# Kernel tuning notes

Hardware: AMD Instinct MI355X
Metric: run time of the kernel (lower is better)

The kernel has to match this reference:

```python
import jax, jax.numpy as jnp
import numpy as np

E = 1024   # embed_dim
H = 16     # num_heads
D = E // H # head_dim = 64
HD2 = D // 2
B = 2
S = 2048


def setup_inputs() -> dict:
    key = jax.random.key(0)
    ks = jax.random.split(key, 12)
    def lin(k, fan_in, fan_out):
        # xavier-uniform-ish init, stored in [in, out] (jax) convention
        lim = float(np.sqrt(6.0 / (fan_in + fan_out)))
        return jax.random.uniform(k, (fan_in, fan_out), jnp.float32, -lim, lim)
    return {
        "query": jax.random.normal(ks[0], (B, S, E), jnp.float32),
        "xi_scale": jax.random.uniform(ks[1], (B,), jnp.float32),
        "Wq": lin(ks[2], E, E), "bq": jnp.zeros((E,), jnp.float32),
        "Wk": lin(ks[3], E, E), "bk": jnp.zeros((E,), jnp.float32),
        "Wv": lin(ks[4], E, E), "bv": jnp.zeros((E,), jnp.float32),
        "Wo": lin(ks[5], E, E), "bo": jnp.zeros((E,), jnp.float32),
        "enc_w1": lin(ks[6], 1, HD2), "enc_b1": jnp.zeros((HD2,), jnp.float32),
        "ln_g": jnp.ones((HD2,), jnp.float32), "ln_b": jnp.zeros((HD2,), jnp.float32),
        "enc_w2": lin(ks[7], HD2, D), "enc_b2": jnp.zeros((D,), jnp.float32),
        "scale_gating": jnp.ones((H,), jnp.float32),
    }


def reference(query, xi_scale, Wq, bq, Wk, bk, Wv, bv, Wo, bo,
              enc_w1, enc_b1, ln_g, ln_b, enc_w2, enc_b2, scale_gating):
    b, s, e = query.shape
    h, d = H, e // H
    # --- scale adaptation: xi -> Linear -> LayerNorm -> GELU -> Linear ---
    x = xi_scale[:, None] @ enc_w1 + enc_b1                  # [B, D/2]
    mu = x.mean(-1, keepdims=True)
    var = ((x - mu) ** 2).mean(-1, keepdims=True)
    x = (x - mu) / jnp.sqrt(var + 1e-5) * ln_g + ln_b
    x = jax.nn.gelu(x, approximate=False)
    xe = x @ enc_w2 + enc_b2                                 # [B, D]
    adapt = 1.0 + jax.nn.sigmoid(scale_gating)[None, :, None] * xe[:, None, :]  # [B, H, D]
    # --- projections (self-attention: key = value = query) ---
    q = (query @ Wq + bq).reshape(b, s, h, d).transpose(0, 2, 1, 3) * adapt[:, :, None, :]
    k = (query @ Wk + bk).reshape(b, s, h, d).transpose(0, 2, 1, 3) * adapt[:, :, None, :]
    v = (query @ Wv + bv).reshape(b, s, h, d).transpose(0, 2, 1, 3)
    # --- explicit QK^T / sqrt(d) -> softmax -> V ---
    inv_scale = 1.0 / float(np.sqrt(d))
    scores = jnp.einsum('bhqd,bhkd->bhqk', q, k) * inv_scale  # [B, H, S, S]
    attn = jax.nn.softmax(scores, axis=-1)
    out = jnp.einsum('bhqk,bhkd->bhqd', attn, v)              # [B, H, S, D]
    out = out.transpose(0, 2, 1, 3).reshape(b, s, e)
    return out @ Wo + bo
```

## Files before the change

kernel.cpp:

```cpp
#include <hip/hip_runtime.h>

typedef __bf16 bf16;
typedef __attribute__((ext_vector_type(8))) __bf16 bf16x8;
typedef __attribute__((ext_vector_type(4))) float f32x4;
typedef __attribute__((ext_vector_type(16))) float f32x16;
typedef unsigned int u32;

#define MFMA16(a, b, c) __builtin_amdgcn_mfma_f32_16x16x32_bf16((a), (b), (c), 0, 0, 0)
#define MFMA32(a, b, c) __builtin_amdgcn_mfma_f32_32x32x16_bf16((a), (b), (c), 0, 0, 0)

#define BB 2
#define SS 2048
#define EE 1024
#define HH 16
#define DD 64
#define MM (BB * SS)

__device__ inline f32x4 zero4() {
    f32x4 z; z.x = 0.f; z.y = 0.f; z.z = 0.f; z.w = 0.f; return z;
}

__device__ __forceinline__ void gload16(const bf16* g, bf16* l) {
    __builtin_amdgcn_global_load_lds(
        (const __attribute__((address_space(1))) u32*)(const void*)g,
        (__attribute__((address_space(3))) u32*)(void*)l,
        16, 0, 0);
}

__device__ __forceinline__ u32 pkbf(float a, float b) {
    union { __bf16 h; unsigned short s; } ua, ub;
    ua.h = (__bf16)a; ub.h = (__bf16)b;
    return (u32)ua.s | ((u32)ub.s << 16);
}

__global__ __launch_bounds__(256) void prep_kernel(
    const float* __restrict__ query, bf16* __restrict__ qc,
    const float* __restrict__ s0, const float* __restrict__ s1,
    const float* __restrict__ s2, const float* __restrict__ s3,
    bf16* __restrict__ d0, bf16* __restrict__ d1,
    bf16* __restrict__ d2, bf16* __restrict__ d3,
    const float* __restrict__ xi, const float* __restrict__ w1,
    const float* __restrict__ b1, const float* __restrict__ lng,
    const float* __restrict__ lnb, const float* __restrict__ w2,
    const float* __restrict__ b2, const float* __restrict__ gate,
    float* __restrict__ adapt) {
    __shared__ bf16 tile[64 * 72];
    const int bid = blockIdx.x;
    const int t = threadIdx.x;

    if (bid < 2048) {
        const int i = (bid * 256 + t) * 8;
        float4 a = *(const float4*)(query + i);
        float4 b = *(const float4*)(query + i + 4);
        bf16 tmp[8];
        tmp[0] = (bf16)a.x; tmp[1] = (bf16)a.y; tmp[2] = (bf16)a.z; tmp[3] = (bf16)a.w;
        tmp[4] = (bf16)b.x; tmp[5] = (bf16)b.y; tmp[6] = (bf16)b.z; tmp[7] = (bf16)b.w;
        *(uint4*)(qc + i) = *(uint4*)tmp;
    } else if (bid < 3072) {
        const int m = (bid - 2048) >> 8;
        const int idx0 = (bid - 2048) & 255;
        const float* W = (m == 0) ? s0 : (m == 1) ? s1 : (m == 2) ? s2 : s3;
        bf16* Wt = (m == 0) ? d0 : (m == 1) ? d1 : (m == 2) ? d2 : d3;
        const int k0 = (idx0 >> 4) * 64, n0 = (idx0 & 15) * 64;
#pragma unroll
        for (int i = 0; i < 2; ++i) {
            int idx = i * 256 + t;
            int r = idx >> 3, c = (idx & 7) * 8;
            float4 a = *(const float4*)(W + (k0 + r) * EE + n0 + c);
            float4 b = *(const float4*)(W + (k0 + r) * EE + n0 + c + 4);
            bf16 tmp[8];
            tmp[0] = (bf16)a.x; tmp[1] = (bf16)a.y; tmp[2] = (bf16)a.z; tmp[3] = (bf16)a.w;
            tmp[4] = (bf16)b.x; tmp[5] = (bf16)b.y; tmp[6] = (bf16)b.z; tmp[7] = (bf16)b.w;
            *(uint4*)(tile + r * 72 + c) = *(uint4*)tmp;
        }
        __syncthreads();
#pragma unroll
        for (int i = 0; i < 2; ++i) {
            int idx = i * 256 + t;
            int n = idx >> 3, kc = (idx & 7) * 8;
            bf16 tmp[8];
#pragma unroll
            for (int j = 0; j < 8; ++j) tmp[j] = tile[(kc + j) * 72 + n];
            *(uint4*)(Wt + (n0 + n) * EE + k0 + kc) = *(uint4*)tmp;
        }
    } else {
        const int b = bid - 3072;
        float* xs = (float*)tile;
        if (t < 64) {
            const float xiv = xi[b];
            float xv = 0.f;
            if (t < 32) xv = xiv * w1[t] + b1[t];
            float sm = xv;
            for (int off = 1; off < 32; off <<= 1) sm += __shfl_xor(sm, off);
            const float mu = sm * (1.f / 32.f);
            float dv = (t < 32) ? (xv - mu) : 0.f;
            float s2 = dv * dv;
            for (int off = 1; off < 32; off <<= 1) s2 += __shfl_xor(s2, off);
            const float var = s2 * (1.f / 32.f);
            if (t < 32) {
                float xn = (xv - mu) * rsqrtf(var + 1e-5f) * lng[t] + lnb[t];
                float ge = 0.5f * xn * (1.f + erff(xn * 0.70710678118654752f));
                xs[t] = ge;
            }
        }
        __syncthreads();
        if (t < 64) {
            float acc = b2[t];
            for (int j = 0; j < 32; ++j) acc += xs[j] * w2[j * DD + t];
            for (int h = 0; h < HH; ++h) {
                float sg = 1.f / (1.f + __expf(-gate[h]));
                adapt[(b * HH + h) * DD + t] = 1.f + sg * acc;
            }
        }
    }
}

__global__ __launch_bounds__(256, 3) void gemm_qkv(
    const bf16* __restrict__ Aq, const bf16* __restrict__ Bqk,
    const bf16* __restrict__ Av,
    const float* __restrict__ bias, const float* __restrict__ bias2,
    const float* __restrict__ bias3, const float* __restrict__ adapt,
    bf16* __restrict__ outqk, bf16* __restrict__ outvt) {
    __shared__ bf16 As[2 * 128 * 32];
    __shared__ bf16 Bs[2 * 128 * 32];

    const int t = threadIdx.x;
    const int w = t >> 6, lane = t & 63;
    const int mrow = lane & 15, quad = lane >> 4;
    const int wm = (w & 1) * 64, wn = (w >> 1) * 64;

    int md, bx, by;
    const bf16 *Ap, *Bp;
    int bid = blockIdx.x;
    if (bid < 512) { md = 5; bx = bid & 31; by = bid >> 5; Ap = Aq; Bp = Bqk; }
    else { md = 4; bid -= 512; bx = bid & 7; by = bid >> 3; Ap = Av; Bp = Aq; }
    const int m0 = bx * 128, n0 = by * 128;

    f32x4 acc[4][4];
#pragma unroll
    for (int i = 0; i < 4; ++i)
#pragma unroll
        for (int j = 0; j < 4; ++j) acc[i][j] = zero4();

    const int dr = lane >> 2;
    const int dcg = ((lane & 3) ^ (dr & 3)) * 8;
    const bf16* Ag = Ap + (size_t)(m0 + w * 16 + dr) * EE + dcg;
    const bf16* Bg = Bp + (size_t)(n0 + w * 16 + dr) * EE + dcg;
    bf16* Al = As + (w * 16) * 32;
    bf16* Bl = Bs + (w * 16) * 32;

    gload16(Ag, Al);
    gload16(Ag + 64 * EE, Al + 64 * 32);
    gload16(Bg, Bl);
    gload16(Bg + 64 * EE, Bl + 64 * 32);

    for (int kt = 0; kt < 32; ++kt) {
        __syncthreads();
        if (kt < 31) {
            const int kn = (kt + 1) * 32;
            const int nb = (kt + 1) & 1;
            gload16(Ag + kn, Al + nb * 4096);
            gload16(Ag + 64 * EE + kn, Al + nb * 4096 + 64 * 32);
            gload16(Bg + kn, Bl + nb * 4096);
            gload16(Bg + 64 * EE + kn, Bl + nb * 4096 + 64 * 32);
        }
        const bf16* Ab = As + (kt & 1) * 4096;
        const bf16* Bb = Bs + (kt & 1) * 4096;
        const int sw = (quad ^ (mrow & 3)) * 8;
        bf16x8 af[4], bfr[4];
#pragma unroll
        for (int i = 0; i < 4; ++i)
            af[i] = *(const bf16x8*)(Ab + (wm + i * 16 + mrow) * 32 + sw);
#pragma unroll
        for (int j = 0; j < 4; ++j)
            bfr[j] = *(const bf16x8*)(Bb + (wn + j * 16 + mrow) * 32 + sw);
#pragma unroll
        for (int i = 0; i < 4; ++i)
#pragma unroll
            for (int j = 0; j < 4; ++j)
                acc[i][j] = MFMA16(af[i], bfr[j], acc[i][j]);
    }

#pragma unroll
    for (int i = 0; i < 4; ++i) {
#pragma unroll
        for (int j = 0; j < 4; ++j) {
            const int col = n0 + wn + j * 16 + mrow;
#pragma unroll
            for (int r = 0; r < 4; ++r) {
                const int row = m0 + wm + i * 16 + quad * 4 + r;
                float v = acc[i][j][r];
                if (md == 4) {
                    v += bias3[row];
                    const int h = row >> 6, d = row & 63;
                    const int b = col >> 11, s = col & (SS - 1);
                    outvt[(((b * HH + h) * DD + d) * SS) + s] = (bf16)v;
                } else {
                    const int m2 = col >> 10;
                    const int cl = col & 1023;
                    const int h = cl >> 6, d = cl & 63;
                    const int b = row >> 11, s = row & (SS - 1);
                    v += (m2 ? bias2[cl] : bias[cl]);
                    v *= adapt[(b * HH + h) * DD + d];
                    if (!m2) v *= 0.18033688011113811f;
                    outqk[(size_t)m2 * MM * EE + ((b * HH + h) * SS + s) * DD + d] = (bf16)v;
                }
            }
        }
    }
}

__global__ __launch_bounds__(256, 3) void gemm_o(
    const bf16* __restrict__ A, const bf16* __restrict__ Bt,
    const float* __restrict__ bias, float* __restrict__ outf) {
    __shared__ bf16 As[2 * 128 * 64];
    __shared__ bf16 Bs[2 * 64 * 64];

    const int t = threadIdx.x;
    const int w = t >> 6, lane = t & 63;
    const int mrow = lane & 15, quad = lane >> 4;
    const int m0 = blockIdx.x * 128, n0 = blockIdx.y * 64;

    f32x4 acc[2][4];
#pragma unroll
    for (int i = 0; i < 2; ++i)
#pragma unroll
        for (int j = 0; j < 4; ++j) acc[i][j] = zero4();

    const int grow = lane >> 3;
    const int gsw = ((lane & 7) ^ grow) * 8;
    const bf16* Ag = A + (size_t)(m0 + w * 32 + grow) * EE + gsw;
    const bf16* Bg = Bt + (size_t)(n0 + w * 16 + grow) * EE + gsw;
    bf16* Al = As + (w * 32) * 64;
    bf16* Bl = Bs + (w * 16) * 64;

#pragma unroll
    for (int i = 0; i < 4; ++i) gload16(Ag + i * 8 * EE, Al + i * 8 * 64);
#pragma unroll
    for (int i = 0; i < 2; ++i) gload16(Bg + i * 8 * EE, Bl + i * 8 * 64);

    for (int kt = 0; kt < 16; ++kt) {
        __syncthreads();
        if (kt < 15) {
            const int kn = (kt + 1) * 64;
            const int nb = (kt + 1) & 1;
#pragma unroll
            for (int i = 0; i < 4; ++i)
                gload16(Ag + i * 8 * EE + kn, Al + nb * 8192 + i * 8 * 64);
#pragma unroll
            for (int i = 0; i < 2; ++i)
                gload16(Bg + i * 8 * EE + kn, Bl + nb * 4096 + i * 8 * 64);
        }
        const bf16* Ab = As + (kt & 1) * 8192;
        const bf16* Bb = Bs + (kt & 1) * 4096;
#pragma unroll
        for (int ks = 0; ks < 2; ++ks) {
            const int cg = ks * 4 + quad;
            const int sw = (cg ^ (mrow & 7)) * 8;
            bf16x8 af[2], bfr[4];
#pragma unroll
            for (int mi = 0; mi < 2; ++mi)
                af[mi] = *(const bf16x8*)(Ab + (w * 32 + mi * 16 + mrow) * 64 + sw);
#pragma unroll
            for (int nj = 0; nj < 4; ++nj)
                bfr[nj] = *(const bf16x8*)(Bb + (nj * 16 + mrow) * 64 + sw);
#pragma unroll
            for (int mi = 0; mi < 2; ++mi)
#pragma unroll
                for (int nj = 0; nj < 4; ++nj)
                    acc[mi][nj] = MFMA16(af[mi], bfr[nj], acc[mi][nj]);
        }
    }

#pragma unroll
    for (int mi = 0; mi < 2; ++mi) {
#pragma unroll
        for (int nj = 0; nj < 4; ++nj) {
            const int col = n0 + nj * 16 + mrow;
#pragma unroll
            for (int r = 0; r < 4; ++r) {
                const int row = m0 + w * 32 + mi * 16 + quad * 4 + r;
                outf[row * EE + col] = acc[mi][nj][r] + bias[col];
            }
        }
    }
}

__global__ __launch_bounds__(256, 2) void attn_kernel(
    const bf16* __restrict__ q, const bf16* __restrict__ k,
    const bf16* __restrict__ vt, bf16* __restrict__ o0, bf16* __restrict__ o1,
    float* __restrict__ lws) {
    __shared__ bf16 lds[16896];
    bf16* Ks = lds;
    bf16* Vs = lds + 8192;

    const int t = threadIdx.x;
    const int w = t >> 6, lane = t & 63;
    const int q32 = lane & 31, h = lane >> 5;
    const int split = blockIdx.x >> 8;
    const int rest = blockIdx.x & 255;
    const int bh = rest >> 3;
    const int qb = rest & 7;
    const int qr0 = qb * 256 + w * 64;

    bf16x8 qf[2][4];
#pragma unroll
    for (int qi = 0; qi < 2; ++qi)
#pragma unroll
        for (int c = 0; c < 4; ++c)
            qf[qi][c] = *(const bf16x8*)(q + (size_t)(bh * SS + qr0 + qi * 32 + q32) * DD +
                                         c * 16 + h * 8);

    f32x16 oacc[2][2];
#pragma unroll
    for (int qi = 0; qi < 2; ++qi)
#pragma unroll
        for (int mf = 0; mf < 2; ++mf)
#pragma unroll
            for (int i = 0; i < 16; ++i) oacc[qi][mf][i] = 0.f;
    float lsum[2] = {0.f, 0.f};

    const int dr = lane >> 3;
    const int dcg = ((lane & 7) ^ dr) * 8;
    const bf16* kg = k + (size_t)bh * SS * DD;
    const bf16* vg = vt + (size_t)bh * DD * SS;
    const bf16* kgl = kg + (size_t)dr * DD + dcg;
    const bf16* vgl = vg + (size_t)(w * 16 + dr) * SS + dcg;

    const int ktbeg = split * (SS / 128), ktend = ktbeg + (SS / 128);

#pragma unroll
    for (int i = 0; i < 2; ++i) {
        const int rb = w * 16 + i * 8;
        gload16(kgl + (size_t)(ktbeg * 64 + rb) * DD, Ks + rb * 64);
        gload16(vgl + (size_t)(i * 8) * SS + ktbeg * 64, Vs + rb * 64);
    }

    for (int kt = ktbeg; kt < ktend; ++kt) {
        __syncthreads();
        if (kt < ktend - 1) {
            const int nb = (kt + 1) & 1;
#pragma unroll
            for (int i = 0; i < 2; ++i) {
                const int rb = w * 16 + i * 8;
                gload16(kgl + (size_t)((kt + 1) * 64 + rb) * DD, Ks + nb * 4096 + rb * 64);
                gload16(vgl + (size_t)(i * 8) * SS + (kt + 1) * 64, Vs + nb * 4096 + rb * 64);
            }
        }
        const bf16* Kb = Ks + (kt & 1) * 4096;
        const bf16* Vb = Vs + (kt & 1) * 4096;

        f32x16 st[2][2];
#pragma unroll
        for (int qi = 0; qi < 2; ++qi)
#pragma unroll
            for (int mf = 0; mf < 2; ++mf)
#pragma unroll
                for (int i = 0; i < 16; ++i) st[qi][mf][i] = 0.f;
#pragma unroll
        for (int c = 0; c < 4; ++c) {
            const int sw = ((2 * c + h) ^ (q32 & 7)) * 8;
#pragma unroll
            for (int mf = 0; mf < 2; ++mf) {
                bf16x8 kf = *(const bf16x8*)(Kb + (mf * 32 + q32) * 64 + sw);
#pragma unroll
                for (int qi = 0; qi < 2; ++qi)
                    st[qi][mf] = MFMA32(kf, qf[qi][c], st[qi][mf]);
            }
        }

        u32 P32[2][2][8];
#pragma unroll
        for (int qi = 0; qi < 2; ++qi)
#pragma unroll
            for (int mf = 0; mf < 2; ++mf)
#pragma unroll
                for (int rp = 0; rp < 8; ++rp) {
                    float pa = __builtin_amdgcn_exp2f(st[qi][mf][2 * rp]);
                    float pb = __builtin_amdgcn_exp2f(st[qi][mf][2 * rp + 1]);
                    lsum[qi] += pa + pb;
                    P32[qi][mf][rp] = pkbf(pa, pb);
                }

#pragma unroll
        for (int c = 0; c < 4; ++c) {
            const int mfs = c >> 1;
            const int ro = (c & 1) * 4;
            union { u32 u[4]; bf16x8 v; } pb[2];
#pragma unroll
            for (int qi = 0; qi < 2; ++qi) {
                u32 vA0 = P32[qi][mfs][ro + 0], vA1 = P32[qi][mfs][ro + 1];
                u32 vB0 = P32[qi][mfs][ro + 2], vB1 = P32[qi][mfs][ro + 3];
                u32 prep0 = h ? vA0 : vB0;
                u32 prep1 = h ? vA1 : vB1;
                u32 sh0 = __shfl_xor(prep0, 32);
                u32 sh1 = __shfl_xor(prep1, 32);
                pb[qi].u[0] = h ? sh0 : vA0;
                pb[qi].u[1] = h ? sh1 : vA1;
                pb[qi].u[2] = h ? vB0 : sh0;
                pb[qi].u[3] = h ? vB1 : sh1;
            }
            const int sw = ((2 * c + h) ^ (q32 & 7)) * 8;
#pragma unroll
            for (int mf = 0; mf < 2; ++mf) {
                bf16x8 vf = *(const bf16x8*)(Vb + (mf * 32 + q32) * 64 + sw);
#pragma unroll
                for (int qi = 0; qi < 2; ++qi)
                    oacc[qi][mf] = MFMA32(vf, pb[qi].v, oacc[qi][mf]);
            }
        }
    }

    lsum[0] += __shfl_xor(lsum[0], 32);
    lsum[1] += __shfl_xor(lsum[1], 32);

    __syncthreads();
    bf16* ob = lds + w * 4224;
#pragma unroll
    for (int qi = 0; qi < 2; ++qi)
#pragma unroll
        for (int mf = 0; mf < 2; ++mf)
#pragma unroll
            for (int rp = 0; rp < 8; ++rp) {
                const int d = 32 * mf + 2 * (rp & 1) + 8 * (rp >> 1) + 4 * h;
                *(u32*)(ob + (qi * 32 + q32) * 66 + d) =
                    pkbf(oacc[qi][mf][2 * rp], oacc[qi][mf][2 * rp + 1]);
            }
    __builtin_amdgcn_s_waitcnt(0);

    bf16* op = split ? o1 : o0;
    const int b = bh >> 4, head = bh & 15;
    const int half = lane & 1;
#pragma unroll
    for (int p = 0; p < 2; ++p) {
        const int r = p * 32 + (lane >> 1);
#pragma unroll
        for (int i = 0; i < 4; ++i) {
            bf16x8 val = *(const bf16x8*)(ob + r * 66 + half * 32 + i * 8);
            *(bf16x8*)(op + (size_t)(b * SS + qr0 + r) * EE + head * DD +
                       half * 32 + i * 8) = val;
        }
    }
    if (lane < 32) {
#pragma unroll
        for (int qi = 0; qi < 2; ++qi)
            lws[split * (32 * SS) + bh * SS + qr0 + qi * 32 + q32] = lsum[qi];
    }
}

__global__ __launch_bounds__(256) void combine_kernel(
    const bf16* __restrict__ p1, const float* __restrict__ lws,
    bf16* __restrict__ o) {
    const int i = (blockIdx.x * 256 + threadIdx.x) * 8;
    const int b = i >> 21, s = (i >> 10) & (SS - 1), h = (i >> 6) & 15;
    const int li = (b * HH + h) * SS + s;
    const float inv = 1.f / (lws[li] + lws[32 * SS + li]);
    uint4 u0 = *(const uint4*)(o + i);
    uint4 u1 = *(const uint4*)(p1 + i);
    bf16 a0[8], a1[8], res[8];
    *(uint4*)a0 = u0; *(uint4*)a1 = u1;
#pragma unroll
    for (int j = 0; j < 8; ++j) res[j] = (bf16)(((float)a0[j] + (float)a1[j]) * inv);
    *(uint4*)(o + i) = *(uint4*)res;
}

extern "C" void kernel_launch(void* const* d_in, const int* in_sizes, int n_in,
                              void* d_out, int out_size, void* d_ws, size_t ws_size,
                              hipStream_t stream) {
    const float* query = (const float*)d_in[0];
    const float* xi    = (const float*)d_in[1];
    const float* Wq = (const float*)d_in[2];  const float* bq = (const float*)d_in[3];
    const float* Wk = (const float*)d_in[4];  const float* bk = (const float*)d_in[5];
    const float* Wv = (const float*)d_in[6];  const float* bv = (const float*)d_in[7];
    const float* Wo = (const float*)d_in[8];  const float* bo = (const float*)d_in[9];
    const float* ew1 = (const float*)d_in[10]; const float* eb1 = (const float*)d_in[11];
    const float* lng = (const float*)d_in[12]; const float* lnb = (const float*)d_in[13];
    const float* ew2 = (const float*)d_in[14]; const float* eb2 = (const float*)d_in[15];
    const float* gate = (const float*)d_in[16];
    float* out = (float*)d_out;

    char* ws = (char*)d_ws;
    const size_t SZ = (size_t)MM * EE * sizeof(bf16);
    bf16* queryc = (bf16*)(ws);
    bf16* p0     = (bf16*)(ws);
    bf16* qws    = (bf16*)(ws + SZ);
    bf16* kws    = (bf16*)(ws + 2 * SZ);
    bf16* wqT    = (bf16*)(ws + 3 * SZ);
    bf16* wkT    = (bf16*)(ws + 3 * SZ + 2097152);
    bf16* wvT    = (bf16*)(ws + 3 * SZ + 2 * 2097152);
    bf16* woT    = (bf16*)(ws + 3 * SZ + 3 * 2097152);
    float* adaptws = (float*)(ws + 4 * SZ);
    float* lws   = (float*)(ws + 4 * SZ + 8192);
    bf16* vtws   = (bf16*)d_out;
    bf16* p1     = (bf16*)((char*)d_out + SZ);

    prep_kernel<<<3074, 256, 0, stream>>>(query, queryc, Wq, Wk, Wv, Wo,
                                          wqT, wkT, wvT, woT,
                                          xi, ew1, eb1, lng, lnb, ew2, eb2, gate,
                                          adaptws);

    gemm_qkv<<<768, 256, 0, stream>>>(queryc, wqT, wvT, bq, bk, bv, adaptws,
                                      qws, vtws);

    attn_kernel<<<512, 256, 0, stream>>>(qws, kws, vtws, p0, p1, lws);
    combine_kernel<<<MM * EE / (256 * 8), 256, 0, stream>>>(p1, lws, p0);

    gemm_o<<<dim3(MM / 128, EE / 64), 256, 0, stream>>>(p0, woT, bo, out);
}
```

Measured before the change: 219.0 us.

## Double KV tile to 128 keys per stage, halving barriers and loop iterations

The attention kernel now stages 128 keys per iteration instead of 64. LDS doubles to 64KB, and V uses a new 16-chunk XOR swizzle over 128-wide rows. Each stage is processed as two 64-key halves, so there are half as many __syncthreads and prefetch issues per key, and each load is larger. The larger LDS footprint may cut occupancy below the 2 blocks per CU implied by launch bounds, and the epilogue's reuse of LDS is unchanged.

```diff
diff --git a/kernel.cpp b/kernel.cpp
--- a/kernel.cpp
+++ b/kernel.cpp
@@ -290,9 +290,9 @@
     const bf16* __restrict__ q, const bf16* __restrict__ k,
     const bf16* __restrict__ vt, bf16* __restrict__ o0, bf16* __restrict__ o1,
     float* __restrict__ lws) {
-    __shared__ bf16 lds[16896];
+    __shared__ bf16 lds[32768];
     bf16* Ks = lds;
-    bf16* Vs = lds + 8192;
+    bf16* Vs = lds + 16384;
 
     const int t = threadIdx.x;
     const int w = t >> 6, lane = t & 63;
@@ -320,20 +320,23 @@
             for (int i = 0; i < 16; ++i) oacc[qi][mf][i] = 0.f;
     float lsum[2] = {0.f, 0.f};
 
-    const int dr = lane >> 3;
-    const int dcg = ((lane & 7) ^ dr) * 8;
+    const int kdr = lane >> 3;
+    const int kdc = ((lane & 7) ^ kdr) * 8;
+    const int vdr = lane >> 4;
+    const int vlc = lane & 15;
+
     const bf16* kg = k + (size_t)bh * SS * DD;
     const bf16* vg = vt + (size_t)bh * DD * SS;
-    const bf16* kgl = kg + (size_t)dr * DD + dcg;
-    const bf16* vgl = vg + (size_t)(w * 16 + dr) * SS + dcg;
-
-    const int ktbeg = split * (SS / 128), ktend = ktbeg + (SS / 128);
-
-#pragma unroll
-    for (int i = 0; i < 2; ++i) {
-        const int rb = w * 16 + i * 8;
-        gload16(kgl + (size_t)(ktbeg * 64 + rb) * DD, Ks + rb * 64);
-        gload16(vgl + (size_t)(i * 8) * SS + ktbeg * 64, Vs + rb * 64);
+
+    const int ktbeg = split * 8, ktend = ktbeg + 8;
+
+#pragma unroll
+    for (int i = 0; i < 4; ++i) {
+        const int krb = w * 32 + i * 8;
+        gload16(kg + (size_t)(ktbeg * 128 + krb + kdr) * DD + kdc, Ks + krb * 64);
+        const int vrb = w * 16 + i * 4;
+        gload16(vg + (size_t)(vrb + vdr) * SS + ktbeg * 128 + ((vlc ^ (i * 4 + vdr)) * 8),
+                Vs + vrb * 128);
     }
 
     for (int kt = ktbeg; kt < ktend; ++kt) {
@@ -341,72 +344,82 @@
         if (kt < ktend - 1) {
             const int nb = (kt + 1) & 1;
 #pragma unroll
-            for (int i = 0; i < 2; ++i) {
-                const int rb = w * 16 + i * 8;
-                gload16(kgl + (size_t)((kt + 1) * 64 + rb) * DD, Ks + nb * 4096 + rb * 64);
-                gload16(vgl + (size_t)(i * 8) * SS + (kt + 1) * 64, Vs + nb * 4096 + rb * 64);
-            }
-        }
-        const bf16* Kb = Ks + (kt & 1) * 4096;
-        const bf16* Vb = Vs + (kt & 1) * 4096;
-
-        f32x16 st[2][2];
-#pragma unroll
-        for (int qi = 0; qi < 2; ++qi)
-#pragma unroll
-            for (int mf = 0; mf < 2; ++mf)
-#pragma unroll
-                for (int i = 0; i < 16; ++i) st[qi][mf][i] = 0.f;
-#pragma unroll
-        for (int c = 0; c < 4; ++c) {
-            const int sw = ((2 * c + h) ^ (q32 & 7)) * 8;
-#pragma unroll
-            for (int mf = 0; mf < 2; ++mf) {
-                bf16x8 kf = *(const bf16x8*)(Kb + (mf * 32 + q32) * 64 + sw);
-#pragma unroll
-                for (int qi = 0; qi < 2; ++qi)
-                    st[qi][mf] = MFMA32(kf, qf[qi][c], st[qi][mf]);
-            }
-        }
-
-        u32 P32[2][2][8];
-#pragma unroll
-        for (int qi = 0; qi < 2; ++qi)
-#pragma unroll
-            for (int mf = 0; mf < 2; ++mf)
-#pragma unroll
-                for (int rp = 0; rp < 8; ++rp) {
-                    float pa = __builtin_amdgcn_exp2f(st[qi][mf][2 * rp]);
-                    float pb = __builtin_amdgcn_exp2f(st[qi][mf][2 * rp + 1]);
-                    lsum[qi] += pa + pb;
-                    P32[qi][mf][rp] = pkbf(pa, pb);
+            for (int i = 0; i < 4; ++i) {
+                const int krb = w * 32 + i * 8;
+                gload16(kg + (size_t)((kt + 1) * 128 + krb + kdr) * DD + kdc,
+                        Ks + nb * 8192 + krb * 64);
+                const int vrb = w * 16 + i * 4;
+                gload16(vg + (size_t)(vrb + vdr) * SS + (kt + 1) * 128 +
+                        ((vlc ^ (i * 4 + vdr)) * 8),
+                        Vs + nb * 8192 + vrb * 128);
+            }
+        }
+        const bf16* Kb = Ks + (kt & 1) * 8192;
+        const bf16* Vb = Vs + (kt & 1) * 8192;
+
+#pragma unroll
+        for (int kh = 0; kh < 2; ++kh) {
+            const bf16* Kh = Kb + kh * 64 * 64;
+
+            f32x16 st[2][2];
+#pragma unroll
+            for (int qi = 0; qi < 2; ++qi)
+#pragma unroll
+                for (int mf = 0; mf < 2; ++mf)
+#pragma unroll
+                    for (int i = 0; i < 16; ++i) st[qi][mf][i] = 0.f;
+#pragma unroll
+            for (int c = 0; c < 4; ++c) {
+                const int sw = ((2 * c + h) ^ (q32 & 7)) * 8;
+#pragma unroll
+                for (int mf = 0; mf < 2; ++mf) {
+                    bf16x8 kf = *(const bf16x8*)(Kh + (mf * 32 + q32) * 64 + sw);
+#pragma unroll
+                    for (int qi = 0; qi < 2; ++qi)
+                        st[qi][mf] = MFMA32(kf, qf[qi][c], st[qi][mf]);
                 }
-
-#pragma unroll
-        for (int c = 0; c < 4; ++c) {
-            const int mfs = c >> 1;
-            const int ro = (c & 1) * 4;
-            union { u32 u[4]; bf16x8 v; } pb[2];
-#pragma unroll
-            for (int qi = 0; qi < 2; ++qi) {
-                u32 vA0 = P32[qi][mfs][ro + 0], vA1 = P32[qi][mfs][ro + 1];
-                u32 vB0 = P32[qi][mfs][ro + 2], vB1 = P32[qi][mfs][ro + 3];
-                u32 prep0 = h ? vA0 : vB0;
-                u32 prep1 = h ? vA1 : vB1;
-                u32 sh0 = __shfl_xor(prep0, 32);
-                u32 sh1 = __shfl_xor(prep1, 32);
-                pb[qi].u[0] = h ? sh0 : vA0;
-                pb[qi].u[1] = h ? sh1 : vA1;
-                pb[qi].u[2] = h ? vB0 : sh0;
-                pb[qi].u[3] = h ? vB1 : sh1;
-            }
-            const int sw = ((2 * c + h) ^ (q32 & 7)) * 8;
-#pragma unroll
-            for (int mf = 0; mf < 2; ++mf) {
-                bf16x8 vf = *(const bf16x8*)(Vb + (mf * 32 + q32) * 64 + sw);
-#pragma unroll
-                for (int qi = 0; qi < 2; ++qi)
-                    oacc[qi][mf] = MFMA32(vf, pb[qi].v, oacc[qi][mf]);
+            }
+
+            u32 P32[2][2][8];
+#pragma unroll
+            for (int qi = 0; qi < 2; ++qi)
+#pragma unroll
+                for (int mf = 0; mf < 2; ++mf)
+#pragma unroll
+                    for (int rp = 0; rp < 8; ++rp) {
+                        float pa = __builtin_amdgcn_exp2f(st[qi][mf][2 * rp]);
+                        float pb = __builtin_amdgcn_exp2f(st[qi][mf][2 * rp + 1]);
+                        lsum[qi] += pa + pb;
+                        P32[qi][mf][rp] = pkbf(pa, pb);
+                    }
+
+#pragma unroll
+            for (int c = 0; c < 4; ++c) {
+                const int mfs = c >> 1;
+                const int ro = (c & 1) * 4;
+                union { u32 u[4]; bf16x8 v; } pb[2];
+#pragma unroll
+                for (int qi = 0; qi < 2; ++qi) {
+                    u32 vA0 = P32[qi][mfs][ro + 0], vA1 = P32[qi][mfs][ro + 1];
+                    u32 vB0 = P32[qi][mfs][ro + 2], vB1 = P32[qi][mfs][ro + 3];
+                    u32 prep0 = h ? vA0 : vB0;
+                    u32 prep1 = h ? vA1 : vB1;
+                    u32 sh0 = __shfl_xor(prep0, 32);
+                    u32 sh1 = __shfl_xor(prep1, 32);
+                    pb[qi].u[0] = h ? sh0 : vA0;
+                    pb[qi].u[1] = h ? sh1 : vA1;
+                    pb[qi].u[2] = h ? vB0 : sh0;
+                    pb[qi].u[3] = h ? vB1 : sh1;
+                }
+#pragma unroll
+                for (int mf = 0; mf < 2; ++mf) {
+                    const int vrow = mf * 32 + q32;
+                    const int sv = ((8 * kh + 2 * c + h) ^ (vrow & 15)) * 8;
+                    bf16x8 vf = *(const bf16x8*)(Vb + vrow * 128 + sv);
+#pragma unroll
+                    for (int qi = 0; qi < 2; ++qi)
+                        oacc[qi][mf] = MFMA32(vf, pb[qi].v, oacc[qi][mf]);
+                }
             }
         }
     }
```

After: 232.8 us. +6.3%, slower.
